# Kernel tuning notes

Measured on AMD Instinct MI355X. Metric: run time of the kernel, lower is better.

The kernel has to match this reference:

```python
import jax, jax.numpy as jnp
import numpy as np

B, T, D, EXP, K = 4, 2048, 1024, 2, 4
H = D * EXP


def setup_inputs() -> dict:
    key = jax.random.key(0)
    ks = jax.random.split(key, 8)
    x = jax.random.normal(ks[0], (B, T, D), jnp.float32)
    W_in = jax.random.normal(ks[1], (2 * H, D), jnp.float32) * D ** -0.5
    s_conv = 1.0 / np.sqrt(K)  # fan_in = (in_ch/groups)*K = K
    W_conv = jax.random.uniform(ks[2], (H, 1, K), jnp.float32, -s_conv, s_conv)
    b_conv = jax.random.uniform(ks[3], (H,), jnp.float32, -s_conv, s_conv)
    W_gates = jax.random.normal(ks[4], (3 * H, H), jnp.float32) * H ** -0.5
    s_g = 1.0 / np.sqrt(H)
    b_gates = jax.random.uniform(ks[5], (3 * H,), jnp.float32, -s_g, s_g)
    W_out = jax.random.normal(ks[6], (D, H), jnp.float32) * H ** -0.5
    alpha_p = jnp.asarray(1.0, jnp.float32)
    return {"x": x, "W_in": W_in, "W_conv": W_conv, "b_conv": b_conv,
            "W_gates": W_gates, "b_gates": b_gates, "W_out": W_out,
            "alpha_p": alpha_p}


def _scan_combine(c1, c2):
    a1, b1 = c1
    a2, b2 = c2
    return (a1 * a2, a2 * b1 + b2)


def reference(x, W_in, W_conv, b_conv, W_gates, b_gates, W_out, alpha_p):
    # input projection -> gate branch and conv branch, each [B,T,H]
    gi = jnp.einsum('btd,ed->bte', x, W_in)
    gate, u = jnp.split(gi, 2, axis=-1)
    # causal depthwise conv over time (torch pads K-1 both sides then keeps [:T])
    uc = jnp.transpose(u, (0, 2, 1))  # [B,H,T]
    v = jax.lax.conv_general_dilated(
        uc, W_conv, window_strides=(1,), padding=[(K - 1, 0)],
        dimension_numbers=('NCH', 'OIH', 'NCH'), feature_group_count=H)
    v = jnp.transpose(v + b_conv[None, :, None], (0, 2, 1))  # [B,T,H]
    # gates
    g = jnp.einsum('bth,gh->btg', v, W_gates) + b_gates
    f, i, o = jnp.split(g, 3, axis=-1)
    # reversed_sigmoid=True: alpha = sigmoid(-f) ** relu(alpha_p)
    alpha = jax.nn.sigmoid(-f) ** jax.nn.relu(alpha_p)
    xin = jax.nn.sigmoid(i) * v
    # diagonal linear recurrence h_t = alpha_t * h_{t-1} + xin_t via parallel scan
    _, h = jax.lax.associative_scan(_scan_combine, (alpha, xin), axis=1)
    h = jax.nn.sigmoid(o) * h
    return jnp.einsum('bth,dh->btd', jax.nn.gelu(gate, approximate=False) * h, W_out)
```

## Files before the change

### kernel.cpp

```cpp
#include <hip/hip_runtime.h>
#include <hip/hip_bf16.h>
#include <cstdint>
#include <cstddef>

#define B_ 4
#define T_ 2048
#define D_ 1024
#define H_ 2048

typedef __attribute__((ext_vector_type(8))) short s8v;
typedef __attribute__((ext_vector_type(4))) float f4v;

__device__ __forceinline__ float bflo(unsigned int u){ union{unsigned int i;float f;}c; c.i=u<<16; return c.f; }
__device__ __forceinline__ float bfhi(unsigned int u){ union{unsigned int i;float f;}c; c.i=u&0xffff0000u; return c.f; }
__device__ __forceinline__ unsigned short f2bf(float f){
    __hip_bfloat16 h = __float2bfloat16(f);
    union { __hip_bfloat16 h; unsigned short u; } c; c.h = h; return c.u;
}
__device__ __forceinline__ unsigned int pk2(float lo, float hi){
    return (unsigned int)f2bf(lo) | ((unsigned int)f2bf(hi) << 16);
}
__device__ __forceinline__ float sigm(float x){ return 1.f/(1.f+expf(-x)); }
__device__ __forceinline__ void up8(uint4 w, float* r){
    r[0]=bflo(w.x); r[1]=bfhi(w.x); r[2]=bflo(w.y); r[3]=bfhi(w.y);
    r[4]=bflo(w.z); r[5]=bfhi(w.z); r[6]=bflo(w.w); r[7]=bfhi(w.w);
}

__device__ __forceinline__ void gload16(const void* g, void* l){
    __builtin_amdgcn_global_load_lds(
        (const __attribute__((address_space(1))) unsigned int*)g,
        (__attribute__((address_space(3))) unsigned int*)l, 16, 0, 0);
}

__global__ __launch_bounds__(256)
void cvt8(const float* __restrict__ s, unsigned short* __restrict__ d)
{
    size_t i = ((size_t)blockIdx.x*256 + threadIdx.x)*8;
    float4 a = *(const float4*)(s+i), b = *(const float4*)(s+i+4);
    uint4 o; o.x=pk2(a.x,a.y); o.y=pk2(a.z,a.w); o.z=pk2(b.x,b.y); o.w=pk2(b.z,b.w);
    *(uint4*)(d+i)=o;
}

template<int AM, int BM, int EPI>
__global__ __launch_bounds__(256)
void mgemm(const void* __restrict__ Asrc, int lda,
           const void* __restrict__ Bsrc, int K, int N,
           unsigned short* __restrict__ C0, unsigned short* __restrict__ C1,
           unsigned short* __restrict__ C2, float* __restrict__ Cf)
{
    __shared__ unsigned short As[128*64];
    __shared__ unsigned short Bs[128*64];
    const int tid = threadIdx.x;
    const int lane = tid & 63;
    const int wid = tid >> 6;

    const int nwg = gridDim.x * 64;
    const int orig = blockIdx.y * gridDim.x + blockIdx.x;
    const int q = nwg >> 3;
    const int wg = (orig & 7) * q + (orig >> 3);
    const int m0 = (wg & 63) * 128;
    const int n0 = (wg >> 6) * 128;

    const int ar0 = wid * 32;
    const int alr = lane >> 3;
    const int alj = lane & 7;
    const int rr = tid >> 1;
    const int kh = tid & 1;

    const int wm = wid >> 1, wn = wid & 1;
    const int fr = lane & 15, fg = lane >> 4;
    int aoff[4][2], boff[4][2];
#pragma unroll
    for (int m = 0; m < 4; ++m) {
        int row = wm*64 + m*16 + fr;
#pragma unroll
        for (int s = 0; s < 2; ++s)
            aoff[m][s] = row*128 + (((s*4 + fg) ^ (row & 7)) * 16);
    }
#pragma unroll
    for (int n = 0; n < 4; ++n) {
        int row = wn*64 + n*16 + fr;
#pragma unroll
        for (int s = 0; s < 2; ++s)
            boff[n][s] = row*128 + (((s*4 + fg) ^ (row & 7)) * 16);
    }
    const char* Asc = (const char*)As;
    const char* Bsc = (const char*)Bs;

    f4v acc[4][4];
#pragma unroll
    for (int m = 0; m < 4; ++m)
#pragma unroll
        for (int n = 0; n < 4; ++n) { f4v z4 = {0.f,0.f,0.f,0.f}; acc[m][n] = z4; }

    for (int k0 = 0; k0 < K; k0 += 64) {
        if (AM == 1) {
            const unsigned short* Ab = (const unsigned short*)Asrc;
#pragma unroll
            for (int i = 0; i < 4; ++i) {
                int row = ar0 + i*8 + alr;
                int ss = alj ^ alr;
                const char* g = (const char*)(Ab + (size_t)(m0+row)*lda + k0) + ss*16;
                gload16(g, (void*)((char*)As + (ar0 + i*8)*128));
            }
        } else {
            const float* src = (const float*)Asrc + (size_t)(m0+rr)*lda + k0 + kh*32;
            float4 v[8];
#pragma unroll
            for (int i = 0; i < 8; ++i) v[i] = ((const float4*)src)[i];
#pragma unroll
            for (int qd = 0; qd < 4; ++qd) {
                uint4 w;
                w.x = pk2(v[2*qd].x, v[2*qd].y);   w.y = pk2(v[2*qd].z, v[2*qd].w);
                w.z = pk2(v[2*qd+1].x, v[2*qd+1].y); w.w = pk2(v[2*qd+1].z, v[2*qd+1].w);
                int j = (kh*4 + qd) ^ (rr & 7);
                *(uint4*)((char*)As + rr*128 + j*16) = w;
            }
        }
        if (BM == 1) {
            const unsigned short* Bb = (const unsigned short*)Bsrc;
#pragma unroll
            for (int i = 0; i < 4; ++i) {
                int row = ar0 + i*8 + alr;
                int ss = alj ^ alr;
                const char* g = (const char*)(Bb + (size_t)(n0+row)*K + k0) + ss*16;
                gload16(g, (void*)((char*)Bs + (ar0 + i*8)*128));
            }
        } else {
            const float* src = (const float*)Bsrc + (size_t)(n0+rr)*K + k0 + kh*32;
            float4 v[8];
#pragma unroll
            for (int i = 0; i < 8; ++i) v[i] = ((const float4*)src)[i];
#pragma unroll
            for (int qd = 0; qd < 4; ++qd) {
                uint4 w;
                w.x = pk2(v[2*qd].x, v[2*qd].y);   w.y = pk2(v[2*qd].z, v[2*qd].w);
                w.z = pk2(v[2*qd+1].x, v[2*qd+1].y); w.w = pk2(v[2*qd+1].z, v[2*qd+1].w);
                int j = (kh*4 + qd) ^ (rr & 7);
                *(uint4*)((char*)Bs + rr*128 + j*16) = w;
            }
        }
        __syncthreads();
#pragma unroll
        for (int s = 0; s < 2; ++s) {
            s8v a[4], b[4];
#pragma unroll
            for (int m = 0; m < 4; ++m) a[m] = *(const s8v*)(Asc + aoff[m][s]);
#pragma unroll
            for (int n = 0; n < 4; ++n) b[n] = *(const s8v*)(Bsc + boff[n][s]);
#pragma unroll
            for (int m = 0; m < 4; ++m)
#pragma unroll
                for (int n = 0; n < 4; ++n)
                    acc[m][n] = __builtin_amdgcn_mfma_f32_16x16x32_bf16(a[m], b[n], acc[m][n], 0, 0, 0);
        }
        __syncthreads();
    }

    const int cr = (lane >> 4) * 4;
    const int cc = lane & 15;
#pragma unroll
    for (int m = 0; m < 4; ++m) {
        const int grow0 = m0 + wm*64 + m*16 + cr;
#pragma unroll
        for (int n = 0; n < 4; ++n) {
            const int colb = n0 + wn*64 + n*16;
            const int gcol = colb + cc;
            if (EPI == 0) {
#pragma unroll
                for (int j = 0; j < 4; ++j)
                    Cf[(size_t)(grow0+j)*N + gcol] = acc[m][n][j];
            } else if (EPI == 1) {
                unsigned short* dst = (colb < H_) ? C0 : C1;
                const int pc = gcol & (H_-1);
#pragma unroll
                for (int j = 0; j < 4; ++j)
                    dst[(size_t)(grow0+j)*H_ + pc] = f2bf(acc[m][n][j]);
            } else {
                const int plane = colb >> 11;
                unsigned short* dst = (plane == 0) ? C0 : ((plane == 1) ? C1 : C2);
                const int pc = gcol & (H_-1);
#pragma unroll
                for (int j = 0; j < 4; ++j)
                    dst[(size_t)(grow0+j)*H_ + pc] = f2bf(acc[m][n][j]);
            }
        }
    }
}

__global__ __launch_bounds__(256)
void conv8(const unsigned short* __restrict__ u, const float* __restrict__ Wc,
           const float* __restrict__ bc, unsigned short* __restrict__ v)
{
    size_t i8 = ((size_t)blockIdx.x*256 + threadIdx.x) * 8;
    int h = (int)(i8 % H_);
    size_t bt = i8 / H_;
    int t = (int)(bt % T_);
    float w[8][4], acc[8];
#pragma unroll
    for (int j = 0; j < 8; ++j) {
        float4 wr = *(const float4*)(Wc + (h+j)*4);
        w[j][0]=wr.x; w[j][1]=wr.y; w[j][2]=wr.z; w[j][3]=wr.w;
        acc[j] = bc[h+j];
    }
    const unsigned short* up = u + bt*H_ + h;
#pragma unroll
    for (int k = 0; k < 4; ++k) {
        int dt = 3 - k;
        if (t >= dt) {
            uint4 r = *(const uint4*)(up - (size_t)dt*H_);
            float e[8]; up8(r, e);
#pragma unroll
            for (int j = 0; j < 8; ++j) acc[j] = fmaf(e[j], w[j][k], acc[j]);
        }
    }
    uint4 o;
    o.x = pk2(acc[0],acc[1]); o.y = pk2(acc[2],acc[3]);
    o.z = pk2(acc[4],acc[5]); o.w = pk2(acc[6],acc[7]);
    *(uint4*)(v + i8) = o;
}

__global__ __launch_bounds__(256)
void scan_chunk8(const unsigned short* __restrict__ fp, const unsigned short* __restrict__ ip,
                 const unsigned short* __restrict__ vp,
                 const float* __restrict__ bg, const float* __restrict__ app,
                 float* __restrict__ cA, float* __restrict__ cB, int CT)
{
    int hh = threadIdx.x * 8;
    int c = blockIdx.y, b = blockIdx.z;
    const float ap = fmaxf(app[0], 0.f);
    const bool ap1 = (ap == 1.0f);
    float bf[8], bi[8];
#pragma unroll
    for (int j = 0; j < 8; ++j) { bf[j] = bg[hh+j]; bi[j] = bg[H_+hh+j]; }
    size_t base = ((size_t)b*T_ + (size_t)c*CT)*H_ + hh;
    float A[8], Bv[8];
#pragma unroll
    for (int j=0;j<8;++j){ A[j]=1.f; Bv[j]=0.f; }
    for (int t = 0; t < CT; ++t) {
        float f[8], i8a[8], v[8];
        up8(*(const uint4*)(fp+base), f);
        up8(*(const uint4*)(ip+base), i8a);
        up8(*(const uint4*)(vp+base), v);
#pragma unroll
        for (int j=0;j<8;++j){
            float s = 1.f/(1.f+expf(f[j]+bf[j]));
            float a = ap1 ? s : powf(s, ap);
            float xin = v[j] / (1.f+expf(-(i8a[j]+bi[j])));
            A[j]*=a; Bv[j]=fmaf(a,Bv[j],xin);
        }
        base += H_;
    }
    size_t ci = ((size_t)b*gridDim.y + c)*H_ + hh;
    *(float4*)(cA+ci)   = (float4){A[0],A[1],A[2],A[3]};
    *(float4*)(cA+ci+4) = (float4){A[4],A[5],A[6],A[7]};
    *(float4*)(cB+ci)   = (float4){Bv[0],Bv[1],Bv[2],Bv[3]};
    *(float4*)(cB+ci+4) = (float4){Bv[4],Bv[5],Bv[6],Bv[7]};
}

__global__ __launch_bounds__(256)
void scan_carry8(const float* __restrict__ cA, const float* __restrict__ cB,
                 float* __restrict__ cin, int NC)
{
    int gt = blockIdx.x*256 + threadIdx.x;
    int hh = (gt * 8) % H_;
    int b  = (gt * 8) / H_;
    float h[8];
#pragma unroll
    for (int j=0;j<8;++j) h[j]=0.f;
    for (int c = 0; c < NC; ++c) {
        size_t ci = ((size_t)b*NC + c)*H_ + hh;
        *(float4*)(cin+ci)   = (float4){h[0],h[1],h[2],h[3]};
        *(float4*)(cin+ci+4) = (float4){h[4],h[5],h[6],h[7]};
        float4 a0 = *(const float4*)(cA+ci), a1 = *(const float4*)(cA+ci+4);
        float4 b0 = *(const float4*)(cB+ci), b1 = *(const float4*)(cB+ci+4);
        float a[8]={a0.x,a0.y,a0.z,a0.w,a1.x,a1.y,a1.z,a1.w};
        float x[8]={b0.x,b0.y,b0.z,b0.w,b1.x,b1.y,b1.z,b1.w};
#pragma unroll
        for (int j=0;j<8;++j) h[j] = fmaf(a[j], h[j], x[j]);
    }
}

__global__ __launch_bounds__(256)
void scan_apply8(const unsigned short* __restrict__ fp, const unsigned short* __restrict__ ip,
                 const unsigned short* __restrict__ op, const unsigned short* __restrict__ ga,
                 unsigned short* __restrict__ vz,
                 const float* __restrict__ bg, const float* __restrict__ app,
                 const float* __restrict__ cin, int CT)
{
    int hh = threadIdx.x * 8;
    int c = blockIdx.y, b = blockIdx.z;
    const float ap = fmaxf(app[0], 0.f);
    const bool ap1 = (ap == 1.0f);
    float bf[8], bi[8], bo[8];
#pragma unroll
    for (int j = 0; j < 8; ++j) {
        bf[j] = bg[hh+j]; bi[j] = bg[H_+hh+j]; bo[j] = bg[2*H_+hh+j];
    }
    size_t base = ((size_t)b*T_ + (size_t)c*CT)*H_ + hh;
    size_t ci = ((size_t)b*gridDim.y + c)*H_ + hh;
    float h[8];
    {
        float4 h0 = *(const float4*)(cin+ci), h1 = *(const float4*)(cin+ci+4);
        h[0]=h0.x; h[1]=h0.y; h[2]=h0.z; h[3]=h0.w;
        h[4]=h1.x; h[5]=h1.y; h[6]=h1.z; h[7]=h1.w;
    }
    for (int t = 0; t < CT; ++t) {
        float f[8], i8a[8], o8[8], g[8], v[8], zo[8];
        up8(*(const uint4*)(fp+base), f);
        up8(*(const uint4*)(ip+base), i8a);
        up8(*(const uint4*)(op+base), o8);
        up8(*(const uint4*)(ga+base), g);
        up8(*(const uint4*)(vz+base), v);
#pragma unroll
        for (int j=0;j<8;++j) {
            float s = 1.f/(1.f+expf(f[j]+bf[j]));
            float a = ap1 ? s : powf(s, ap);
            float xin = v[j] / (1.f+expf(-(i8a[j]+bi[j])));
            h[j] = fmaf(a, h[j], xin);
            float so = 1.f/(1.f+expf(-(o8[j]+bo[j])));
            float ge = 0.5f*g[j]*(1.f+erff(g[j]*0.70710678118654752f));
            zo[j] = ge * so * h[j];
        }
        uint4 o;
        o.x = pk2(zo[0],zo[1]); o.y = pk2(zo[2],zo[3]);
        o.z = pk2(zo[4],zo[5]); o.w = pk2(zo[6],zo[7]);
        *(uint4*)(vz + base) = o;
        base += H_;
    }
}

__global__ void zero_out(float* __restrict__ out, size_t n)
{
    for (size_t i = (size_t)blockIdx.x*256 + threadIdx.x; i < n; i += (size_t)gridDim.x*256)
        out[i] = 0.f;
}

extern "C" void kernel_launch(void* const* d_in, const int* in_sizes, int n_in,
                              void* d_out, int out_size, void* d_ws, size_t ws_size,
                              hipStream_t stream)
{
    const float* x       = (const float*)d_in[0];
    const float* W_in    = (const float*)d_in[1];
    const float* W_conv  = (const float*)d_in[2];
    const float* b_conv  = (const float*)d_in[3];
    const float* W_gates = (const float*)d_in[4];
    const float* b_gates = (const float*)d_in[5];
    const float* W_out   = (const float*)d_in[6];
    const float* alpha_p = (const float*)d_in[7];
    float* out = (float*)d_out;

    const size_t plane = (size_t)B_ * T_ * H_;
    unsigned short* gate = (unsigned short*)d_ws;
    unsigned short* fpl  = gate + plane;
    unsigned short* v    = fpl + plane;
    unsigned short* ipl  = v + plane;
    unsigned short* opl  = ipl + plane;
    char* R = (char*)(opl + plane);

    const size_t x_elems  = (size_t)B_*T_*D_;
    const size_t wg_elems = (size_t)3*H_*H_;
    const size_t wi_elems = (size_t)2*H_*D_;
    const size_t wo_elems = (size_t)D_*H_;
    const int NCF = 64;
    const size_t carry_b = 3*(size_t)B_*NCF*H_*4;
    const size_t Rneed = x_elems*2 > carry_b + wo_elems*2 ? x_elems*2 : carry_b + wo_elems*2;
    const size_t need_fast = 5*plane*2 + Rneed;

    if (ws_size >= need_fast && (size_t)out_size*4 >= (wg_elems + wi_elems)*2) {
        unsigned short* wgb  = (unsigned short*)d_out;
        unsigned short* winb = wgb + wg_elems;
        unsigned short* xb   = (unsigned short*)R;
        float* cAp  = (float*)R;
        float* cBp  = cAp + (size_t)B_*NCF*H_;
        float* cinp = cBp + (size_t)B_*NCF*H_;
        unsigned short* woutb = (unsigned short*)(cinp + (size_t)B_*NCF*H_);
        const int CT = T_ / NCF;

        cvt8<<<(unsigned)(x_elems/2048),  256, 0, stream>>>(x, xb);
        cvt8<<<(unsigned)(wi_elems/2048), 256, 0, stream>>>(W_in, winb);
        cvt8<<<(unsigned)(wg_elems/2048), 256, 0, stream>>>(W_gates, wgb);
        mgemm<1,1,1><<<dim3(32,64), 256, 0, stream>>>(
            xb, D_, winb, D_, 2*H_, gate, fpl, nullptr, nullptr);
        conv8<<<(unsigned)(plane/8/256), 256, 0, stream>>>(fpl, W_conv, b_conv, v);
        cvt8<<<(unsigned)(wo_elems/2048), 256, 0, stream>>>(W_out, woutb);
        mgemm<1,1,2><<<dim3(48,64), 256, 0, stream>>>(
            v, H_, wgb, H_, 3*H_, fpl, ipl, opl, nullptr);
        scan_chunk8<<<dim3(1,NCF,B_), 256, 0, stream>>>(fpl, ipl, v, b_gates, alpha_p, cAp, cBp, CT);
        scan_carry8<<<(B_*H_/8)/256, 256, 0, stream>>>(cAp, cBp, cinp, NCF);
        scan_apply8<<<dim3(1,NCF,B_), 256, 0, stream>>>(fpl, ipl, opl, gate, v, b_gates, alpha_p, cinp, CT);
        mgemm<1,1,0><<<dim3(8,64), 256, 0, stream>>>(
            v, H_, woutb, H_, D_, nullptr, nullptr, nullptr, out);
        return;
    }

    float* cAp = (float*)R;
    int NC = 64;
    if (ws_size < 5*plane*2 + 3*(size_t)B_*64*H_*4) {
        NC = 16;
        if (ws_size < 5*plane*2 + 3*(size_t)B_*16*H_*4) {
            zero_out<<<2048, 256, 0, stream>>>(out, (size_t)out_size);
            return;
        }
    }
    const int CT = T_ / NC;
    float* cBp  = cAp + (size_t)B_*NC*H_;
    float* cinp = cBp + (size_t)B_*NC*H_;

    mgemm<0,0,1><<<dim3(32,64), 256, 0, stream>>>(
        x, D_, W_in, D_, 2*H_, gate, fpl, nullptr, nullptr);
    conv8<<<(unsigned)(plane/8/256), 256, 0, stream>>>(fpl, W_conv, b_conv, v);
    mgemm<1,0,2><<<dim3(48,64), 256, 0, stream>>>(
        v, H_, W_gates, H_, 3*H_, fpl, ipl, opl, nullptr);
    scan_chunk8<<<dim3(1,NC,B_), 256, 0, stream>>>(fpl, ipl, v, b_gates, alpha_p, cAp, cBp, CT);
    scan_carry8<<<(B_*H_/8)/256, 256, 0, stream>>>(cAp, cBp, cinp, NC);
    scan_apply8<<<dim3(1,NC,B_), 256, 0, stream>>>(fpl, ipl, opl, gate, v, b_gates, alpha_p, cinp, CT);
    mgemm<1,0,0><<<dim3(8,64), 256, 0, stream>>>(
        v, H_, W_out, H_, D_, nullptr, nullptr, nullptr, out);
}
```

Measured before the change: 643.7 us.

## Remap GEMM tiles per XCD and widen scan parallelism with more chunks

Changes the GEMM workgroup-to-tile mapping so each XCD handles a contiguous group of M tiles, grouped in fours, to improve L2 reuse of the A and B operands. The scan kernels now split H across two 128-thread blocks and the chunk count doubles from 64 to 128, giving more concurrent workgroups on the memory-bound scan passes. The carry kernel switches to one thread per channel for more parallelism. In exchange it uses a larger carry workspace and shorter chunks, which add carry-pass work.

```diff
diff --git a/kernel.cpp b/kernel.cpp
--- a/kernel.cpp
+++ b/kernel.cpp
@@ -54,12 +54,15 @@
     const int lane = tid & 63;
     const int wid = tid >> 6;
 
-    const int nwg = gridDim.x * 64;
-    const int orig = blockIdx.y * gridDim.x + blockIdx.x;
-    const int q = nwg >> 3;
-    const int wg = (orig & 7) * q + (orig >> 3);
-    const int m0 = (wg & 63) * 128;
-    const int n0 = (wg >> 6) * 128;
+    const int nxb = gridDim.x;
+    const int orig = blockIdx.y * nxb + blockIdx.x;
+    const int xcd = orig & 7;
+    const int i = orig >> 3;
+    const int gsz = nxb << 2;
+    const int g = i / gsz;
+    const int r = i - g * gsz;
+    const int n0 = (r >> 2) * 128;
+    const int m0 = (xcd * 8 + g * 4 + (r & 3)) * 128;
 
     const int ar0 = wid * 32;
     const int alr = lane >> 3;
@@ -97,17 +100,17 @@
         if (AM == 1) {
             const unsigned short* Ab = (const unsigned short*)Asrc;
 #pragma unroll
-            for (int i = 0; i < 4; ++i) {
-                int row = ar0 + i*8 + alr;
+            for (int i2 = 0; i2 < 4; ++i2) {
+                int row = ar0 + i2*8 + alr;
                 int ss = alj ^ alr;
-                const char* g = (const char*)(Ab + (size_t)(m0+row)*lda + k0) + ss*16;
-                gload16(g, (void*)((char*)As + (ar0 + i*8)*128));
+                const char* gp = (const char*)(Ab + (size_t)(m0+row)*lda + k0) + ss*16;
+                gload16(gp, (void*)((char*)As + (ar0 + i2*8)*128));
             }
         } else {
             const float* src = (const float*)Asrc + (size_t)(m0+rr)*lda + k0 + kh*32;
             float4 v[8];
 #pragma unroll
-            for (int i = 0; i < 8; ++i) v[i] = ((const float4*)src)[i];
+            for (int i2 = 0; i2 < 8; ++i2) v[i2] = ((const float4*)src)[i2];
 #pragma unroll
             for (int qd = 0; qd < 4; ++qd) {
                 uint4 w;
@@ -120,17 +123,17 @@
         if (BM == 1) {
             const unsigned short* Bb = (const unsigned short*)Bsrc;
 #pragma unroll
-            for (int i = 0; i < 4; ++i) {
-                int row = ar0 + i*8 + alr;
+            for (int i2 = 0; i2 < 4; ++i2) {
+                int row = ar0 + i2*8 + alr;
                 int ss = alj ^ alr;
-                const char* g = (const char*)(Bb + (size_t)(n0+row)*K + k0) + ss*16;
-                gload16(g, (void*)((char*)Bs + (ar0 + i*8)*128));
+                const char* gp = (const char*)(Bb + (size_t)(n0+row)*K + k0) + ss*16;
+                gload16(gp, (void*)((char*)Bs + (ar0 + i2*8)*128));
             }
         } else {
             const float* src = (const float*)Bsrc + (size_t)(n0+rr)*K + k0 + kh*32;
             float4 v[8];
 #pragma unroll
-            for (int i = 0; i < 8; ++i) v[i] = ((const float4*)src)[i];
+            for (int i2 = 0; i2 < 8; ++i2) v[i2] = ((const float4*)src)[i2];
 #pragma unroll
             for (int qd = 0; qd < 4; ++qd) {
                 uint4 w;
@@ -220,13 +223,13 @@
     *(uint4*)(v + i8) = o;
 }
 
-__global__ __launch_bounds__(256)
+__global__ __launch_bounds__(128)
 void scan_chunk8(const unsigned short* __restrict__ fp, const unsigned short* __restrict__ ip,
                  const unsigned short* __restrict__ vp,
                  const float* __restrict__ bg, const float* __restrict__ app,
                  float* __restrict__ cA, float* __restrict__ cB, int CT)
 {
-    int hh = threadIdx.x * 8;
+    int hh = (blockIdx.x * 128 + threadIdx.x) * 8;
     int c = blockIdx.y, b = blockIdx.z;
     const float ap = fmaxf(app[0], 0.f);
     const bool ap1 = (ap == 1.0f);
@@ -259,36 +262,28 @@
 }
 
 __global__ __launch_bounds__(256)
-void scan_carry8(const float* __restrict__ cA, const float* __restrict__ cB,
+void scan_carry1(const float* __restrict__ cA, const float* __restrict__ cB,
                  float* __restrict__ cin, int NC)
 {
-    int gt = blockIdx.x*256 + threadIdx.x;
-    int hh = (gt * 8) % H_;
-    int b  = (gt * 8) / H_;
-    float h[8];
-#pragma unroll
-    for (int j=0;j<8;++j) h[j]=0.f;
+    int idx = blockIdx.x*256 + threadIdx.x;
+    int b  = idx >> 11;
+    int hh = idx & (H_-1);
+    float h = 0.f;
     for (int c = 0; c < NC; ++c) {
         size_t ci = ((size_t)b*NC + c)*H_ + hh;
-        *(float4*)(cin+ci)   = (float4){h[0],h[1],h[2],h[3]};
-        *(float4*)(cin+ci+4) = (float4){h[4],h[5],h[6],h[7]};
-        float4 a0 = *(const float4*)(cA+ci), a1 = *(const float4*)(cA+ci+4);
-        float4 b0 = *(const float4*)(cB+ci), b1 = *(const float4*)(cB+ci+4);
-        float a[8]={a0.x,a0.y,a0.z,a0.w,a1.x,a1.y,a1.z,a1.w};
-        float x[8]={b0.x,b0.y,b0.z,b0.w,b1.x,b1.y,b1.z,b1.w};
-#pragma unroll
-        for (int j=0;j<8;++j) h[j] = fmaf(a[j], h[j], x[j]);
-    }
-}
-
-__global__ __launch_bounds__(256)
+        cin[ci] = h;
+        h = fmaf(cA[ci], h, cB[ci]);
+    }
+}
+
+__global__ __launch_bounds__(128)
 void scan_apply8(const unsigned short* __restrict__ fp, const unsigned short* __restrict__ ip,
                  const unsigned short* __restrict__ op, const unsigned short* __restrict__ ga,
                  unsigned short* __restrict__ vz,
                  const float* __restrict__ bg, const float* __restrict__ app,
                  const float* __restrict__ cin, int CT)
 {
-    int hh = threadIdx.x * 8;
+    int hh = (blockIdx.x * 128 + threadIdx.x) * 8;
     int c = blockIdx.y, b = blockIdx.z;
     const float ap = fmaxf(app[0], 0.f);
     const bool ap1 = (ap == 1.0f);
@@ -362,7 +357,7 @@
     const size_t wg_elems = (size_t)3*H_*H_;
     const size_t wi_elems = (size_t)2*H_*D_;
     const size_t wo_elems = (size_t)D_*H_;
-    const int NCF = 64;
+    const int NCF = 128;
     const size_t carry_b = 3*(size_t)B_*NCF*H_*4;
     const size_t Rneed = x_elems*2 > carry_b + wo_elems*2 ? x_elems*2 : carry_b + wo_elems*2;
     const size_t need_fast = 5*plane*2 + Rneed;
@@ -386,17 +381,17 @@
         cvt8<<<(unsigned)(wo_elems/2048), 256, 0, stream>>>(W_out, woutb);
         mgemm<1,1,2><<<dim3(48,64), 256, 0, stream>>>(
             v, H_, wgb, H_, 3*H_, fpl, ipl, opl, nullptr);
-        scan_chunk8<<<dim3(1,NCF,B_), 256, 0, stream>>>(fpl, ipl, v, b_gates, alpha_p, cAp, cBp, CT);
-        scan_carry8<<<(B_*H_/8)/256, 256, 0, stream>>>(cAp, cBp, cinp, NCF);
-        scan_apply8<<<dim3(1,NCF,B_), 256, 0, stream>>>(fpl, ipl, opl, gate, v, b_gates, alpha_p, cinp, CT);
+        scan_chunk8<<<dim3(2,NCF,B_), 128, 0, stream>>>(fpl, ipl, v, b_gates, alpha_p, cAp, cBp, CT);
+        scan_carry1<<<(B_*H_)/256, 256, 0, stream>>>(cAp, cBp, cinp, NCF);
+        scan_apply8<<<dim3(2,NCF,B_), 128, 0, stream>>>(fpl, ipl, opl, gate, v, b_gates, alpha_p, cinp, CT);
         mgemm<1,1,0><<<dim3(8,64), 256, 0, stream>>>(
             v, H_, woutb, H_, D_, nullptr, nullptr, nullptr, out);
         return;
     }
 
     float* cAp = (float*)R;
-    int NC = 64;
-    if (ws_size < 5*plane*2 + 3*(size_t)B_*64*H_*4) {
+    int NC = 128;
+    if (ws_size < 5*plane*2 + 3*(size_t)B_*128*H_*4) {
         NC = 16;
         if (ws_size < 5*plane*2 + 3*(size_t)B_*16*H_*4) {
             zero_out<<<2048, 256, 0, stream>>>(out, (size_t)out_size);
@@ -412,9 +407,9 @@
     conv8<<<(unsigned)(plane/8/256), 256, 0, stream>>>(fpl, W_conv, b_conv, v);
     mgemm<1,0,2><<<dim3(48,64), 256, 0, stream>>>(
         v, H_, W_gates, H_, 3*H_, fpl, ipl, opl, nullptr);
-    scan_chunk8<<<dim3(1,NC,B_), 256, 0, stream>>>(fpl, ipl, v, b_gates, alpha_p, cAp, cBp, CT);
-    scan_carry8<<<(B_*H_/8)/256, 256, 0, stream>>>(cAp, cBp, cinp, NC);
-    scan_apply8<<<dim3(1,NC,B_), 256, 0, stream>>>(fpl, ipl, opl, gate, v, b_gates, alpha_p, cinp, CT);
+    scan_chunk8<<<dim3(2,NC,B_), 128, 0, stream>>>(fpl, ipl, v, b_gates, alpha_p, cAp, cBp, CT);
+    scan_carry1<<<(B_*H_)/256, 256, 0, stream>>>(cAp, cBp, cinp, NC);
+    scan_apply8<<<dim3(2,NC,B_), 128, 0, stream>>>(fpl, ipl, opl, gate, v, b_gates, alpha_p, cinp, CT);
     mgemm<1,0,0><<<dim3(8,64), 256, 0, stream>>>(
         v, H_, W_out, H_, D_, nullptr, nullptr, nullptr, out);
 }
```

After: 577.5 us. 1.11x faster.
